# Kernel optimization log

Measured on AMD Instinct MI355X. Metric: run time of the kernel, lower is better.

The kernel has to match this reference:

```python
import jax, jax.numpy as jnp
import numpy as np


def setup_inputs() -> dict:
    key = jax.random.key(0)
    kq, kk, kv = jax.random.split(key, 3)
    bs, K, t, d, vocab = 32, 16, 4, 64, 8192
    q = jax.random.normal(kq, (bs, K, t, d), dtype=jnp.float32)
    k = jax.random.normal(kk, (bs, vocab, t, d), dtype=jnp.float32)
    v = jax.random.normal(kv, (bs, vocab, t, d), dtype=jnp.float32)
    return {"q": q, "k": k, "v": v}


def reference(q, k, v):
    # q: (bs,K,t,d), k/v: (bs,vocab,t,d)
    scale = q.shape[-1] ** -0.5
    # logits/attn: (bs,t,K,vocab) -- matches torch transpose(1,2) then matmul
    logits = jnp.einsum('bktd,bvtd->btkv', q * scale, k)
    attn = jax.nn.softmax(logits, axis=-1)
    # per-row argmax over vocab for every t (vectorized over the t loop)
    tokens = jnp.swapaxes(jnp.argmax(attn, axis=-1), 1, 2)  # (bs,K,t)
    # weighted sum over vocab, back to (bs,K,t,d)
    out = jnp.einsum('btkv,bvtd->bktd', attn, v)
    return (out, tokens)
```

## Files before the change

kernel.cpp:

```cpp
#include <hip/hip_runtime.h>
#include <math.h>


#define BSZ 32
#define KQ  16
#define TT  4
#define DD  64
#define VOC 8192
#define TR  16
#define NW  4
#define PART 1088
#define FIXM 20.0f

#define BR4(k) ((((k)&1)<<3)|(((k)&2)<<1)|(((k)&4)>>1)|(((k)&8)>>3))

__device__ __forceinline__ void gl_lds16(const float* g, float* l) {
    __builtin_amdgcn_global_load_lds(
        (const __attribute__((address_space(1))) void*)g,
        (__attribute__((address_space(3))) void*)l, 16, 0, 0);
}
__device__ __forceinline__ float fxor1(float x) {
    return __int_as_float(__builtin_amdgcn_update_dpp(
        0, __float_as_int(x), 0xB1 , 0xF, 0xF, true));
}
__device__ __forceinline__ float fxor2(float x) {
    return __int_as_float(__builtin_amdgcn_update_dpp(
        0, __float_as_int(x), 0x4E , 0xF, 0xF, true));
}
#define XSWZ4(x) __int_as_float(__builtin_amdgcn_ds_swizzle(__float_as_int(x), 0x101F))
#define XSWZ8(x) __int_as_float(__builtin_amdgcn_ds_swizzle(__float_as_int(x), 0x201F))

__global__ __launch_bounds__(256, 2)
void bat_main(const float* __restrict__ Q, const float* __restrict__ Kp,
              const float* __restrict__ Vp, float* __restrict__ ws, int NC)
{
    __shared__ __align__(16) float kvK[4 * 1024];
    __shared__ __align__(16) float ps[NW * 64];
    __shared__ float lS[NW * KQ], bvS[NW * KQ], biS[NW * KQ];

    const int tid  = threadIdx.x;
    const int w    = tid >> 6;
    const int lane = tid & 63;
    const int o    = lane & 15;
    const int r    = lane >> 4;
    const int kkq  = BR4(o);
    const int bid  = blockIdx.x;
    const int c    = bid % NC;
    const int t    = (bid / NC) % TT;
    const int b    = bid / (NC * TT);
    const int CHUNK = VOC / NC;
    const int NT    = CHUNK / TR;
    const int row0  = c * CHUNK;

    float4 qr[KQ];
    {
        const float4* qg = reinterpret_cast<const float4*>(Q + (size_t)b * KQ * TT * DD);
#pragma unroll
        for (int kk2 = 0; kk2 < KQ; ++kk2) {
            float4 qv = qg[(kk2 * TT + t) * (DD / 4) + o];
            qv.x *= 0.125f; qv.y *= 0.125f; qv.z *= 0.125f; qv.w *= 0.125f;
            qr[kk2] = qv;
        }
    }

    const size_t rstride = TT * DD;
    const float* gK = Kp + ((size_t)b * VOC + row0 + w * 4 + r) * rstride
                         + (size_t)t * DD + (o << 2);
    const float* gV = Vp + ((size_t)b * VOC + row0 + w * 4) * rstride
                         + (size_t)t * DD + lane;

    auto SK = [&](int it) {
        gl_lds16(gK + (size_t)it * TR * rstride, kvK + (it & 3) * 1024 + w * 256);
    };
#define SV(it, d0, d1, d2, d3)                                  \
    {                                                           \
        const float* vbp = gV + (size_t)(it) * TR * rstride;    \
        d0 = vbp[0];                                            \
        d1 = vbp[rstride];                                      \
        d2 = vbp[2 * rstride];                                  \
        d3 = vbp[3 * rstride];                                  \
    }

    float O[KQ];
#pragma unroll
    for (int i = 0; i < KQ; ++i) O[i] = 0.f;
    float l0 = 0.f, bv0 = -INFINITY;
    int   bi0 = 0;
    float va0, va1, va2, va3, vb0, vb1, vb2, vb3;
    float4 fA, fB;

    auto C = [&](int it, const float4& fuse, float4& fpre,
                 float v0, float v1, float v2, float v3) {
        float acc[KQ];
#pragma unroll
        for (int kk2 = 0; kk2 < KQ; ++kk2) {
            const float4 q = qr[kk2];
            float s = q.x * fuse.x;
            s = fmaf(q.y, fuse.y, s);
            s = fmaf(q.z, fuse.z, s);
            s = fmaf(q.w, fuse.w, s);
            acc[kk2] = s;
        }
        float nn[8];
#pragma unroll
        for (int j = 0; j < 8; ++j) {
            const float sA = fxor1(acc[j]);
            const float sB = fxor1(acc[j + 8]);
            nn[j] = (o & 1) ? (acc[j + 8] + sB) : (acc[j] + sA);
        }
        float mm[4];
#pragma unroll
        for (int j = 0; j < 4; ++j) {
            const float sA = fxor2(nn[j]);
            const float sB = fxor2(nn[j + 4]);
            mm[j] = (o & 2) ? (nn[j + 4] + sB) : (nn[j] + sA);
        }
        float p0, p1;
        {
            const float sA = XSWZ4(mm[0]);
            const float sB = XSWZ4(mm[2]);
            const float sC = XSWZ4(mm[1]);
            const float sD = XSWZ4(mm[3]);
            p0 = (o & 4) ? (mm[2] + sB) : (mm[0] + sA);
            p1 = (o & 4) ? (mm[3] + sD) : (mm[1] + sC);
        }
        float f;
        {
            const float sA = XSWZ8(p0);
            const float sB = XSWZ8(p1);
            f = (o & 8) ? (p1 + sB) : (p0 + sA);
        }

        const int rowAbs = row0 + it * TR + w * 4 + r;
        if (f > bv0) { bv0 = f; bi0 = rowAbs; }
        const float p = __expf(f - FIXM);
        l0 += p;
        ps[w * 64 + r * 16 + kkq] = p;

        fpre = *reinterpret_cast<const float4*>(
            kvK + ((it + 1) & 3) * 1024 + w * 256 + lane * 4);

#pragma unroll
        for (int rr = 0; rr < 4; ++rr) {
            const float vv = (rr == 0) ? v0 : (rr == 1) ? v1 : (rr == 2) ? v2 : v3;
            const float* pp = ps + w * 64 + rr * 16;
            const float4 pa = *reinterpret_cast<const float4*>(pp + 0);
            const float4 pb = *reinterpret_cast<const float4*>(pp + 4);
            const float4 pc = *reinterpret_cast<const float4*>(pp + 8);
            const float4 pd = *reinterpret_cast<const float4*>(pp + 12);
            O[0]  = fmaf(pa.x, vv, O[0]);
            O[1]  = fmaf(pa.y, vv, O[1]);
            O[2]  = fmaf(pa.z, vv, O[2]);
            O[3]  = fmaf(pa.w, vv, O[3]);
            O[4]  = fmaf(pb.x, vv, O[4]);
            O[5]  = fmaf(pb.y, vv, O[5]);
            O[6]  = fmaf(pb.z, vv, O[6]);
            O[7]  = fmaf(pb.w, vv, O[7]);
            O[8]  = fmaf(pc.x, vv, O[8]);
            O[9]  = fmaf(pc.y, vv, O[9]);
            O[10] = fmaf(pc.z, vv, O[10]);
            O[11] = fmaf(pc.w, vv, O[11]);
            O[12] = fmaf(pd.x, vv, O[12]);
            O[13] = fmaf(pd.y, vv, O[13]);
            O[14] = fmaf(pd.z, vv, O[14]);
            O[15] = fmaf(pd.w, vv, O[15]);
        }
    };

    SK(0); SK(1); SV(0, va0, va1, va2, va3); SK(2); SV(1, vb0, vb1, vb2, vb3);
    {
        SK(3);
        asm volatile("s_waitcnt vmcnt(6)" ::: "memory");
        __builtin_amdgcn_sched_barrier(0);
        fA = *reinterpret_cast<const float4*>(kvK + w * 256 + lane * 4);
        C(0, fA, fB, va0, va1, va2, va3);
        SV(2, va0, va1, va2, va3);
    }
    for (int it = 1; it + 4 < NT; it += 2) {
        SK(it + 3);
        asm volatile("s_waitcnt vmcnt(6)" ::: "memory");
        __builtin_amdgcn_sched_barrier(0);
        C(it, fB, fA, vb0, vb1, vb2, vb3);
        SV(it + 2, vb0, vb1, vb2, vb3);
        SK(it + 4);
        asm volatile("s_waitcnt vmcnt(6)" ::: "memory");
        __builtin_amdgcn_sched_barrier(0);
        C(it + 1, fA, fB, va0, va1, va2, va3);
        SV(it + 3, va0, va1, va2, va3);
    }
    asm volatile("s_waitcnt vmcnt(5)" ::: "memory");
    __builtin_amdgcn_sched_barrier(0);
    C(NT - 3, fB, fA, vb0, vb1, vb2, vb3);
    SV(NT - 1, vb0, vb1, vb2, vb3);
    asm volatile("s_waitcnt vmcnt(4)" ::: "memory");
    __builtin_amdgcn_sched_barrier(0);
    C(NT - 2, fA, fB, va0, va1, va2, va3);
    asm volatile("s_waitcnt vmcnt(0)" ::: "memory");
    __builtin_amdgcn_sched_barrier(0);
    C(NT - 1, fB, fA, vb0, vb1, vb2, vb3);

    l0 += __shfl_xor(l0, 16, 64);
    l0 += __shfl_xor(l0, 32, 64);
#pragma unroll
    for (int s = 16; s <= 32; s <<= 1) {
        const float ov = __shfl_xor(bv0, s, 64);
        const int   oi = __shfl_xor(bi0, s, 64);
        if (ov > bv0 || (ov == bv0 && oi < bi0)) { bv0 = ov; bi0 = oi; }
    }

    __syncthreads();
    float* mO = kvK;
#pragma unroll
    for (int okk = 0; okk < KQ; ++okk) mO[(w * KQ + okk) * 64 + lane] = O[okk];
    if (r == 0) {
        lS[w * KQ + kkq]  = l0;
        bvS[w * KQ + kkq] = bv0;
        biS[w * KQ + kkq] = (float)bi0;
    }
    __syncthreads();

    float* wp = ws + (((size_t)(b * TT + t)) * NC + c) * PART;
    {
        const int mk = tid >> 4, d4 = tid & 15;
        float4 os = make_float4(0.f, 0.f, 0.f, 0.f);
#pragma unroll
        for (int ww = 0; ww < NW; ++ww) {
            const float4 ov = *reinterpret_cast<const float4*>(&mO[(ww * KQ + mk) * 64 + d4 * 4]);
            os.x += ov.x; os.y += ov.y; os.z += ov.z; os.w += ov.w;
        }
        *reinterpret_cast<float4*>(wp + mk * 64 + d4 * 4) = os;
    }
    if (tid < KQ) {
        float L = 0.f;
#pragma unroll
        for (int ww = 0; ww < NW; ++ww) L += lS[ww * KQ + tid];
        float BV = -INFINITY, BI = 0.f;
#pragma unroll
        for (int ww = 0; ww < NW; ++ww) {
            const float v   = bvS[ww * KQ + tid];
            const float ixf = biS[ww * KQ + tid];
            if (v > BV || (v == BV && ixf < BI)) { BV = v; BI = ixf; }
        }
        wp[1024 + tid] = L;
        wp[1040 + tid] = BV;
        wp[1056 + tid] = BI;
    }
}

__global__ __launch_bounds__(256)
void bat_combine(const float* __restrict__ ws, float* __restrict__ out, int NC)
{
    const int bt  = blockIdx.x;
    const int b   = bt >> 2, t = bt & 3;
    const int tid = threadIdx.x;
    const int kk  = tid >> 4;
    const int d4  = tid & 15;
    const float* base = ws + (size_t)bt * NC * PART;

    float4 O = make_float4(0.f, 0.f, 0.f, 0.f);
    float  L = 0.f;
    for (int c = 0; c < NC; ++c) {
        const float* wp = base + (size_t)c * PART;
        const float4 oc = *reinterpret_cast<const float4*>(wp + kk * 64 + d4 * 4);
        O.x += oc.x; O.y += oc.y; O.z += oc.z; O.w += oc.w;
        L   += wp[1024 + kk];
    }
    const float inv = 1.f / L;
    const size_t oidx = (((size_t)b * KQ + kk) * TT + t) * DD + d4 * 4;
    *reinterpret_cast<float4*>(&out[oidx]) =
        make_float4(O.x * inv, O.y * inv, O.z * inv, O.w * inv);

    if (d4 == 0) {
        float BV = -INFINITY, BI = 0.f;
        for (int c = 0; c < NC; ++c) {
            const float* wp = base + (size_t)c * PART;
            const float v   = wp[1040 + kk];
            const float ixf = wp[1056 + kk];
            if (v > BV || (v == BV && ixf < BI)) { BV = v; BI = ixf; }
        }
        out[(size_t)BSZ * KQ * TT * DD + (size_t)(b * KQ + kk) * TT + t] = BI;
    }
}

extern "C" void kernel_launch(void* const* d_in, const int* in_sizes, int n_in,
                              void* d_out, int out_size, void* d_ws, size_t ws_size,
                              hipStream_t stream)
{
    const float* q = (const float*)d_in[0];
    const float* k = (const float*)d_in[1];
    const float* v = (const float*)d_in[2];
    float* out = (float*)d_out;
    float* ws  = (float*)d_ws;

    int NC = 8;
    while (NC > 1 && (size_t)BSZ * TT * NC * PART * sizeof(float) > ws_size) NC >>= 1;

    bat_main<<<dim3(BSZ * TT * NC), dim3(256), 0, stream>>>(q, k, v, ws, NC);
    bat_combine<<<dim3(BSZ * TT), dim3(256), 0, stream>>>(ws, out, NC);
}
```

Before: 130.6 us.

## Software-pipeline softmax-probability and PV accumulation stages with double-buffered LDS

Splits the per-tile compute into a logits/probability stage and a P·V accumulation stage. The PV for tile it-1 now runs after the logits for tile it, using a double-buffered LDS probability array. This hides the LDS write-then-read latency of the probabilities within a tile, at the cost of extra LDS space and a reshuffled V prefetch and waitcnt schedule that must stay correct.

```diff
diff --git a/kernel.cpp b/kernel.cpp
--- a/kernel.cpp
+++ b/kernel.cpp
@@ -35,7 +35,7 @@
               const float* __restrict__ Vp, float* __restrict__ ws, int NC)
 {
     __shared__ __align__(16) float kvK[4 * 1024];
-    __shared__ __align__(16) float ps[NW * 64];
+    __shared__ __align__(16) float ps2[2 * NW * 64];
     __shared__ float lS[NW * KQ], bvS[NW * KQ], biS[NW * KQ];
 
     const int tid  = threadIdx.x;
@@ -89,8 +89,7 @@
     float va0, va1, va2, va3, vb0, vb1, vb2, vb3;
     float4 fA, fB;
 
-    auto C = [&](int it, const float4& fuse, float4& fpre,
-                 float v0, float v1, float v2, float v3) {
+    auto CL = [&](int it, const float4& fuse, float4& fpre) {
         float acc[KQ];
 #pragma unroll
         for (int kk2 = 0; kk2 < KQ; ++kk2) {
@@ -135,31 +134,34 @@
         if (f > bv0) { bv0 = f; bi0 = rowAbs; }
         const float p = __expf(f - FIXM);
         l0 += p;
-        ps[w * 64 + r * 16 + kkq] = p;
+        ps2[(it & 1) * (NW * 64) + w * 64 + r * 16 + kkq] = p;
 
         fpre = *reinterpret_cast<const float4*>(
             kvK + ((it + 1) & 3) * 1024 + w * 256 + lane * 4);
-
+    };
+
+    auto PV = [&](int pit, float v0, float v1, float v2, float v3) {
+        const float* pb = ps2 + (pit & 1) * (NW * 64) + w * 64;
 #pragma unroll
         for (int rr = 0; rr < 4; ++rr) {
             const float vv = (rr == 0) ? v0 : (rr == 1) ? v1 : (rr == 2) ? v2 : v3;
-            const float* pp = ps + w * 64 + rr * 16;
+            const float* pp = pb + rr * 16;
             const float4 pa = *reinterpret_cast<const float4*>(pp + 0);
-            const float4 pb = *reinterpret_cast<const float4*>(pp + 4);
-            const float4 pc = *reinterpret_cast<const float4*>(pp + 8);
+            const float4 pc4 = *reinterpret_cast<const float4*>(pp + 8);
+            const float4 pbv = *reinterpret_cast<const float4*>(pp + 4);
             const float4 pd = *reinterpret_cast<const float4*>(pp + 12);
             O[0]  = fmaf(pa.x, vv, O[0]);
             O[1]  = fmaf(pa.y, vv, O[1]);
             O[2]  = fmaf(pa.z, vv, O[2]);
             O[3]  = fmaf(pa.w, vv, O[3]);
-            O[4]  = fmaf(pb.x, vv, O[4]);
-            O[5]  = fmaf(pb.y, vv, O[5]);
-            O[6]  = fmaf(pb.z, vv, O[6]);
-            O[7]  = fmaf(pb.w, vv, O[7]);
-            O[8]  = fmaf(pc.x, vv, O[8]);
-            O[9]  = fmaf(pc.y, vv, O[9]);
-            O[10] = fmaf(pc.z, vv, O[10]);
-            O[11] = fmaf(pc.w, vv, O[11]);
+            O[4]  = fmaf(pbv.x, vv, O[4]);
+            O[5]  = fmaf(pbv.y, vv, O[5]);
+            O[6]  = fmaf(pbv.z, vv, O[6]);
+            O[7]  = fmaf(pbv.w, vv, O[7]);
+            O[8]  = fmaf(pc4.x, vv, O[8]);
+            O[9]  = fmaf(pc4.y, vv, O[9]);
+            O[10] = fmaf(pc4.z, vv, O[10]);
+            O[11] = fmaf(pc4.w, vv, O[11]);
             O[12] = fmaf(pd.x, vv, O[12]);
             O[13] = fmaf(pd.y, vv, O[13]);
             O[14] = fmaf(pd.z, vv, O[14]);
@@ -167,37 +169,44 @@
         }
     };
 
-    SK(0); SK(1); SV(0, va0, va1, va2, va3); SK(2); SV(1, vb0, vb1, vb2, vb3);
-    {
-        SK(3);
-        asm volatile("s_waitcnt vmcnt(6)" ::: "memory");
-        __builtin_amdgcn_sched_barrier(0);
-        fA = *reinterpret_cast<const float4*>(kvK + w * 256 + lane * 4);
-        C(0, fA, fB, va0, va1, va2, va3);
-        SV(2, va0, va1, va2, va3);
-    }
+    SK(0); SK(1); SK(2); SV(0, va0, va1, va2, va3); SK(3);
+    asm volatile("s_waitcnt vmcnt(6)" ::: "memory");
+    __builtin_amdgcn_sched_barrier(0);
+    fA = *reinterpret_cast<const float4*>(kvK + w * 256 + lane * 4);
+    CL(0, fA, fB);
+    SV(1, vb0, vb1, vb2, vb3);
+
     for (int it = 1; it + 4 < NT; it += 2) {
         SK(it + 3);
         asm volatile("s_waitcnt vmcnt(6)" ::: "memory");
         __builtin_amdgcn_sched_barrier(0);
-        C(it, fB, fA, vb0, vb1, vb2, vb3);
-        SV(it + 2, vb0, vb1, vb2, vb3);
+        CL(it, fB, fA);
+        PV(it - 1, va0, va1, va2, va3);
+        SV(it + 1, va0, va1, va2, va3);
         SK(it + 4);
         asm volatile("s_waitcnt vmcnt(6)" ::: "memory");
         __builtin_amdgcn_sched_barrier(0);
-        C(it + 1, fA, fB, va0, va1, va2, va3);
-        SV(it + 3, va0, va1, va2, va3);
+        CL(it + 1, fA, fB);
+        PV(it, vb0, vb1, vb2, vb3);
+        SV(it + 2, vb0, vb1, vb2, vb3);
     }
     asm volatile("s_waitcnt vmcnt(5)" ::: "memory");
     __builtin_amdgcn_sched_barrier(0);
-    C(NT - 3, fB, fA, vb0, vb1, vb2, vb3);
+    CL(NT - 3, fB, fA);
+    PV(NT - 4, va0, va1, va2, va3);
+    SV(NT - 2, va0, va1, va2, va3);
+    asm volatile("s_waitcnt vmcnt(4)" ::: "memory");
+    __builtin_amdgcn_sched_barrier(0);
+    CL(NT - 2, fA, fB);
+    PV(NT - 3, vb0, vb1, vb2, vb3);
     SV(NT - 1, vb0, vb1, vb2, vb3);
     asm volatile("s_waitcnt vmcnt(4)" ::: "memory");
     __builtin_amdgcn_sched_barrier(0);
-    C(NT - 2, fA, fB, va0, va1, va2, va3);
+    CL(NT - 1, fB, fA);
+    PV(NT - 2, va0, va1, va2, va3);
     asm volatile("s_waitcnt vmcnt(0)" ::: "memory");
     __builtin_amdgcn_sched_barrier(0);
-    C(NT - 1, fB, fA, vb0, vb1, vb2, vb3);
+    PV(NT - 1, vb0, vb1, vb2, vb3);
 
     l0 += __shfl_xor(l0, 16, 64);
     l0 += __shfl_xor(l0, 32, 64);
```

Result: slower. 151.5 us (+16.0%).

## Load K rows directly into registers instead of staging through LDS

Applied to the files above, without the earlier changes.

K tiles are now read from global memory straight into float4 registers, double-buffered alongside the V loads, replacing the global_load_lds path and its 4-slot LDS ring. This removes the LDS write and read round trip for K and frees 16KB of shared memory, which could allow more occupancy. The last cross-lane reduction step swaps a ds_swizzle for a DPP row operation, and the first barrier before the epilogue is dropped because the output buffer no longer aliases the K staging area. In exchange the prefetch depth shrinks from four K tiles in flight to two, so the loop may hide memory latency less well.

```diff
diff --git a/kernel.cpp b/kernel.cpp
--- a/kernel.cpp
+++ b/kernel.cpp
@@ -14,11 +14,6 @@
 
 #define BR4(k) ((((k)&1)<<3)|(((k)&2)<<1)|(((k)&4)>>1)|(((k)&8)>>3))
 
-__device__ __forceinline__ void gl_lds16(const float* g, float* l) {
-    __builtin_amdgcn_global_load_lds(
-        (const __attribute__((address_space(1))) void*)g,
-        (__attribute__((address_space(3))) void*)l, 16, 0, 0);
-}
 __device__ __forceinline__ float fxor1(float x) {
     return __int_as_float(__builtin_amdgcn_update_dpp(
         0, __float_as_int(x), 0xB1 , 0xF, 0xF, true));
@@ -27,14 +22,17 @@
     return __int_as_float(__builtin_amdgcn_update_dpp(
         0, __float_as_int(x), 0x4E , 0xF, 0xF, true));
 }
+__device__ __forceinline__ float fxor8(float x) {
+    return __int_as_float(__builtin_amdgcn_update_dpp(
+        0, __float_as_int(x), 0x128 , 0xF, 0xF, true));
+}
 #define XSWZ4(x) __int_as_float(__builtin_amdgcn_ds_swizzle(__float_as_int(x), 0x101F))
-#define XSWZ8(x) __int_as_float(__builtin_amdgcn_ds_swizzle(__float_as_int(x), 0x201F))
 
 __global__ __launch_bounds__(256, 2)
 void bat_main(const float* __restrict__ Q, const float* __restrict__ Kp,
               const float* __restrict__ Vp, float* __restrict__ ws, int NC)
 {
-    __shared__ __align__(16) float kvK[4 * 1024];
+    __shared__ __align__(16) float mOs[NW * KQ * 64];
     __shared__ __align__(16) float ps[NW * 64];
     __shared__ float lS[NW * KQ], bvS[NW * KQ], biS[NW * KQ];
 
@@ -64,14 +62,13 @@
     }
 
     const size_t rstride = TT * DD;
-    const float* gK = Kp + ((size_t)b * VOC + row0 + w * 4 + r) * rstride
-                         + (size_t)t * DD + (o << 2);
+    const float* gKl = Kp + ((size_t)b * VOC + row0 + w * 4 + r) * rstride
+                          + (size_t)t * DD + (o << 2);
     const float* gV = Vp + ((size_t)b * VOC + row0 + w * 4) * rstride
                          + (size_t)t * DD + lane;
 
-    auto SK = [&](int it) {
-        gl_lds16(gK + (size_t)it * TR * rstride, kvK + (it & 3) * 1024 + w * 256);
-    };
+#define LK(it, kd)                                                          \
+    kd = *reinterpret_cast<const float4*>(gKl + (size_t)(it) * TR * rstride);
 #define SV(it, d0, d1, d2, d3)                                  \
     {                                                           \
         const float* vbp = gV + (size_t)(it) * TR * rstride;    \
@@ -87,18 +84,18 @@
     float l0 = 0.f, bv0 = -INFINITY;
     int   bi0 = 0;
     float va0, va1, va2, va3, vb0, vb1, vb2, vb3;
-    float4 fA, fB;
-
-    auto C = [&](int it, const float4& fuse, float4& fpre,
+    float4 kA, kB;
+
+    auto C = [&](int it, const float4& kx,
                  float v0, float v1, float v2, float v3) {
         float acc[KQ];
 #pragma unroll
         for (int kk2 = 0; kk2 < KQ; ++kk2) {
             const float4 q = qr[kk2];
-            float s = q.x * fuse.x;
-            s = fmaf(q.y, fuse.y, s);
-            s = fmaf(q.z, fuse.z, s);
-            s = fmaf(q.w, fuse.w, s);
+            float s = q.x * kx.x;
+            s = fmaf(q.y, kx.y, s);
+            s = fmaf(q.z, kx.z, s);
+            s = fmaf(q.w, kx.w, s);
             acc[kk2] = s;
         }
         float nn[8];
@@ -126,8 +123,8 @@
         }
         float f;
         {
-            const float sA = XSWZ8(p0);
-            const float sB = XSWZ8(p1);
+            const float sA = fxor8(p0);
+            const float sB = fxor8(p1);
             f = (o & 8) ? (p1 + sB) : (p0 + sA);
         }
 
@@ -136,9 +133,6 @@
         const float p = __expf(f - FIXM);
         l0 += p;
         ps[w * 64 + r * 16 + kkq] = p;
-
-        fpre = *reinterpret_cast<const float4*>(
-            kvK + ((it + 1) & 3) * 1024 + w * 256 + lane * 4);
 
 #pragma unroll
         for (int rr = 0; rr < 4; ++rr) {
@@ -167,37 +161,24 @@
         }
     };
 
-    SK(0); SK(1); SV(0, va0, va1, va2, va3); SK(2); SV(1, vb0, vb1, vb2, vb3);
-    {
-        SK(3);
-        asm volatile("s_waitcnt vmcnt(6)" ::: "memory");
+    LK(0, kA); SV(0, va0, va1, va2, va3);
+    LK(1, kB); SV(1, vb0, vb1, vb2, vb3);
+    for (int it = 0; it + 2 < NT; it += 2) {
+        asm volatile("s_waitcnt vmcnt(5)" ::: "memory");
         __builtin_amdgcn_sched_barrier(0);
-        fA = *reinterpret_cast<const float4*>(kvK + w * 256 + lane * 4);
-        C(0, fA, fB, va0, va1, va2, va3);
-        SV(2, va0, va1, va2, va3);
-    }
-    for (int it = 1; it + 4 < NT; it += 2) {
-        SK(it + 3);
-        asm volatile("s_waitcnt vmcnt(6)" ::: "memory");
+        C(it, kA, va0, va1, va2, va3);
+        LK(it + 2, kA); SV(it + 2, va0, va1, va2, va3);
+        asm volatile("s_waitcnt vmcnt(5)" ::: "memory");
         __builtin_amdgcn_sched_barrier(0);
-        C(it, fB, fA, vb0, vb1, vb2, vb3);
-        SV(it + 2, vb0, vb1, vb2, vb3);
-        SK(it + 4);
-        asm volatile("s_waitcnt vmcnt(6)" ::: "memory");
-        __builtin_amdgcn_sched_barrier(0);
-        C(it + 1, fA, fB, va0, va1, va2, va3);
-        SV(it + 3, va0, va1, va2, va3);
+        C(it + 1, kB, vb0, vb1, vb2, vb3);
+        LK(it + 3, kB); SV(it + 3, vb0, vb1, vb2, vb3);
     }
     asm volatile("s_waitcnt vmcnt(5)" ::: "memory");
     __builtin_amdgcn_sched_barrier(0);
-    C(NT - 3, fB, fA, vb0, vb1, vb2, vb3);
-    SV(NT - 1, vb0, vb1, vb2, vb3);
-    asm volatile("s_waitcnt vmcnt(4)" ::: "memory");
-    __builtin_amdgcn_sched_barrier(0);
-    C(NT - 2, fA, fB, va0, va1, va2, va3);
+    C(NT - 2, kA, va0, va1, va2, va3);
     asm volatile("s_waitcnt vmcnt(0)" ::: "memory");
     __builtin_amdgcn_sched_barrier(0);
-    C(NT - 1, fB, fA, vb0, vb1, vb2, vb3);
+    C(NT - 1, kB, vb0, vb1, vb2, vb3);
 
     l0 += __shfl_xor(l0, 16, 64);
     l0 += __shfl_xor(l0, 32, 64);
@@ -208,8 +189,7 @@
         if (ov > bv0 || (ov == bv0 && oi < bi0)) { bv0 = ov; bi0 = oi; }
     }
 
-    __syncthreads();
-    float* mO = kvK;
+    float* mO = mOs;
 #pragma unroll
     for (int okk = 0; okk < KQ; ++okk) mO[(w * KQ + okk) * 64 + lane] = O[okk];
     if (r == 0) {
```

Result: slower. 133.3 us (+2.1%).
